# Performance work log

Measured on AMD Instinct MI355X. Metric: run time of the kernel, lower is better.

## Reference

```python
import jax, jax.numpy as jnp
import numpy as np

MASKED = True


def setup_inputs() -> dict:
    key = jax.random.key(0)
    kq, kk, kv = jax.random.split(key, 3)
    shape = (4, 16, 2048, 64)  # [B, H, S, d]
    q = jax.random.normal(kq, shape, dtype=jnp.float32)
    k = jax.random.normal(kk, shape, dtype=jnp.float32)
    v = jax.random.normal(kv, shape, dtype=jnp.float32)
    return {"q": q, "k": k, "v": v}


def reference(q, k, v):
    d = k.shape[-1]
    scale = 1.0 / jnp.sqrt(jnp.asarray(d, dtype=q.dtype))
    # [B, H, S, S]
    att = jnp.einsum("bhqd,bhkd->bhqk", q, k) * scale
    if MASKED:
        # Faithful to torch source: tril of the scores, then mask where zero
        tri = jnp.tril(att)
        att = jnp.where(tri == 0, -jnp.inf, att)
    att = jax.nn.softmax(att, axis=-1)
    return jnp.einsum("bhqk,bhkd->bhqd", att, v)
```

## Files before the change

kernel.cpp:

```cpp
#include <hip/hip_runtime.h>
#include <hip/hip_bf16.h>

typedef __attribute__((ext_vector_type(8)))  short bf16x8;
typedef __attribute__((ext_vector_type(4)))  float f32x4;
typedef __attribute__((ext_vector_type(16))) float f32x16;
typedef unsigned short ushort_t;

#define S_LEN 2048
#define D_DIM 64
#define FIXED_M 14.0f

#if __has_builtin(__builtin_amdgcn_exp2f)
#define EXP2(x) __builtin_amdgcn_exp2f(x)
#else
#define EXP2(x) __expf((x) * 0.6931471805599453f)
#endif

__device__ __forceinline__ short f2bf(float f) {
  union { float f; unsigned u; } x; x.f = f;
  unsigned r = x.u + 0x7fffu + ((x.u >> 16) & 1u);
  return (short)(r >> 16);
}

__device__ __forceinline__ unsigned cvtpk_bf16(float lo, float hi) {
  unsigned r;
  asm("v_cvt_pk_bf16_f32 %0, %1, %2" : "=v"(r) : "v"(lo), "v"(hi));
  return r;
}

__device__ __forceinline__ void pl32swap(unsigned& a, unsigned& b) {
  asm volatile("v_permlane32_swap_b32 %0, %1" : "+v"(a), "+v"(b));
}

__device__ __forceinline__ void gl_lds16(const ushort_t* g, ushort_t* l) {
  __builtin_amdgcn_global_load_lds(
      (const __attribute__((address_space(1))) unsigned*)g,
      (__attribute__((address_space(3))) unsigned*)l, 16, 0, 0);
}

__global__ void conv_bf16_kernel(const float* __restrict__ in,
                                 ushort_t* __restrict__ out, long n8) {
  long i = (long)blockIdx.x * blockDim.x + threadIdx.x;
  const long stride = (long)gridDim.x * blockDim.x;
  for (; i < n8; i += stride) {
    const float4* p = (const float4*)(in + i * 8);
    float4 a = p[0], b = p[1];
    bf16x8 t;
    t[0]=f2bf(a.x); t[1]=f2bf(a.y); t[2]=f2bf(a.z); t[3]=f2bf(a.w);
    t[4]=f2bf(b.x); t[5]=f2bf(b.y); t[6]=f2bf(b.z); t[7]=f2bf(b.w);
    *(bf16x8*)(out + i * 8) = t;
  }
}

__global__ void transpose_v_kernel(const float* __restrict__ V,
                                   ushort_t* __restrict__ Vt) {
  const int h  = blockIdx.x >> 5;
  const int s0 = (blockIdx.x & 31) * 64;
  const float* Vh = V + (size_t)h * S_LEN * D_DIM;
  ushort_t* Vth   = Vt + (size_t)h * D_DIM * S_LEN;
  __shared__ float tile[64][65];
  const int r  = threadIdx.x >> 2;
  const int c4 = (threadIdx.x & 3) * 16;
#pragma unroll
  for (int j = 0; j < 16; j += 4) {
    float4 x = *(const float4*)(Vh + (size_t)(s0 + r) * D_DIM + c4 + j);
    tile[r][c4 + j + 0] = x.x; tile[r][c4 + j + 1] = x.y;
    tile[r][c4 + j + 2] = x.z; tile[r][c4 + j + 3] = x.w;
  }
  __syncthreads();
  bf16x8 o0, o1;
#pragma unroll
  for (int j = 0; j < 8; ++j) o0[j] = f2bf(tile[c4 + j][r]);
#pragma unroll
  for (int j = 0; j < 8; ++j) o1[j] = f2bf(tile[c4 + 8 + j][r]);
  *(bf16x8*)(Vth + (size_t)r * S_LEN + s0 + c4)     = o0;
  *(bf16x8*)(Vth + (size_t)r * S_LEN + s0 + c4 + 8) = o1;
}

__global__ __launch_bounds__(256, 2)
void flash32_kernel(const float* __restrict__ Qf, const ushort_t* __restrict__ Kb,
                    const ushort_t* __restrict__ Vt, float* __restrict__ Og) {
  const int tid = threadIdx.x;
  const int l   = tid & 63;
  const int wv  = tid >> 6;
  const int hi  = l >> 5;
  const int l31 = l & 31;
  const int l7  = l & 7;
  const int l8  = l >> 3;

  const int bid  = blockIdx.x;
  const int r6   = bid & 63;
  const int head = (r6 & 7) * 8 + (r6 >> 3);
  const int g4   = bid >> 6;
  const int lo2  = g4 & 3;
  const int odd  = (g4 >> 2) & 1;
  const int top  = g4 >> 3;
  const int qidx = odd ? (top * 4 + lo2) : ((15 - top * 4) - lo2);
  const int q0   = qidx * 128;
  const int nt   = 2 * qidx + 2;

  const float*    Qh = Qf + (size_t)head * S_LEN * D_DIM;
  const ushort_t* Kh = Kb + (size_t)head * S_LEN * D_DIM;
  const ushort_t* Vh = Vt + (size_t)head * D_DIM * S_LEN;
  float*          Oh = Og + (size_t)head * S_LEN * D_DIM;

  __shared__ ushort_t smK[2][64 * 64];
  __shared__ ushort_t smV[2][64 * 64];

  const int qrow  = q0 + wv * 32 + l31;
  const int qminw = q0 + wv * 32;

  const int swsrc = (l7 ^ l8) * 8;
  const int rb    = l31 * 64;

#define STAGE_K(T, B) do {                                                 \
    const int kvk_ = (T) * 64;                                             \
    _Pragma("unroll")                                                      \
    for (int u_ = 0; u_ < 2; ++u_) {                                       \
      const int idx_ = wv * 2 + u_;                                        \
      const int row_ = idx_ * 8 + l8;                                      \
      gl_lds16(Kh + (size_t)(kvk_ + row_) * 64 + swsrc,                    \
               &smK[B][idx_ * 512]);                                       \
    }                                                                      \
  } while (0)

#define STAGE_V(T, B) do {                                                 \
    const int kvv_ = (T) * 64;                                             \
    _Pragma("unroll")                                                      \
    for (int u_ = 0; u_ < 2; ++u_) {                                       \
      const int idx_ = wv * 2 + u_;                                        \
      const int d_ = idx_ * 8 + l8;                                        \
      gl_lds16(Vh + (size_t)d_ * S_LEN + kvv_ + swsrc,                     \
               &smV[B][idx_ * 512]);                                       \
    }                                                                      \
  } while (0)

#define VMCNT0() asm volatile("s_waitcnt vmcnt(0)" ::: "memory")

#define QKT(S0, S1, KB) do {                                               \
    _Pragma("unroll")                                                      \
    for (int i = 0; i < 16; ++i) { S0[i] = 0.f; S1[i] = 0.f; }             \
    const ushort_t* kb_ = smK[KB];                                         \
    __builtin_amdgcn_s_setprio(1);                                         \
    _Pragma("unroll")                                                      \
    for (int ks = 0; ks < 4; ++ks) {                                       \
      const int ch = ((ks * 2 + hi) ^ l7) * 8;                             \
      bf16x8 a0 = *(const bf16x8*)(kb_ + rb + ch);                         \
      bf16x8 a1 = *(const bf16x8*)(kb_ + 2048 + rb + ch);                  \
      S0 = __builtin_amdgcn_mfma_f32_32x32x16_bf16(a0, qf[ks], S0, 0, 0, 0); \
      S1 = __builtin_amdgcn_mfma_f32_32x32x16_bf16(a1, qf[ks], S1, 0, 0, 0); \
    }                                                                      \
    __builtin_amdgcn_s_setprio(0);                                         \
  } while (0)

#define SOFTMAX(S0, S1, KV0) do {                                          \
    if ((KV0) + 63 > qminw) {                                              \
      _Pragma("unroll")                                                    \
      for (int r = 0; r < 16; ++r) {                                       \
        const int crow = (r & 3) + 8 * (r >> 2) + 4 * hi;                  \
        if ((KV0) + crow > qrow)      S0[r] = -INFINITY;                   \
        if ((KV0) + 32 + crow > qrow) S1[r] = -INFINITY;                   \
      }                                                                    \
    }                                                                      \
    _Pragma("unroll")                                                      \
    for (int i = 0; i < 16; ++i) S0[i] = EXP2(S0[i] - FIXED_M);            \
    _Pragma("unroll")                                                      \
    for (int i = 0; i < 16; ++i) S1[i] = EXP2(S1[i] - FIXED_M);            \
    float b8[8];                                                           \
    _Pragma("unroll")                                                      \
    for (int i = 0; i < 8; ++i)                                            \
      b8[i] = (S0[i] + S0[i+8]) + (S1[i] + S1[i+8]);                       \
    _Pragma("unroll")                                                      \
    for (int i = 0; i < 4; ++i) b8[i] += b8[i+4];                          \
    l_run += (b8[0] + b8[2]) + (b8[1] + b8[3]);                            \
    _Pragma("unroll")                                                      \
    for (int ks = 0; ks < 4; ++ks) {                                       \
      const int r0 = (ks & 1) * 8;                                         \
      unsigned w0, w1, w2, w3;                                             \
      if (ks < 2) {                                                        \
        w0 = cvtpk_bf16(S0[r0+0], S0[r0+1]); w2 = cvtpk_bf16(S0[r0+4], S0[r0+5]); \
        w1 = cvtpk_bf16(S0[r0+2], S0[r0+3]); w3 = cvtpk_bf16(S0[r0+6], S0[r0+7]); \
      } else {                                                             \
        w0 = cvtpk_bf16(S1[r0+0], S1[r0+1]); w2 = cvtpk_bf16(S1[r0+4], S1[r0+5]); \
        w1 = cvtpk_bf16(S1[r0+2], S1[r0+3]); w3 = cvtpk_bf16(S1[r0+6], S1[r0+7]); \
      }                                                                    \
      pl32swap(w0, w2); pl32swap(w1, w3);                                  \
      union { unsigned u[4]; bf16x8 v; } pu_;                              \
      pu_.u[0] = w0; pu_.u[1] = w1; pu_.u[2] = w2; pu_.u[3] = w3;          \
      pw[ks] = pu_.v;                                                      \
    }                                                                      \
  } while (0)

#define PV(VB) do {                                                        \
    const ushort_t* vb_ = smV[VB];                                         \
    __builtin_amdgcn_s_setprio(1);                                         \
    _Pragma("unroll")                                                      \
    for (int ks = 0; ks < 4; ++ks) {                                       \
      const int ch = ((ks * 2 + hi) ^ l7) * 8;                             \
      bf16x8 va  = *(const bf16x8*)(vb_ + rb + ch);                        \
      bf16x8 vB2 = *(const bf16x8*)(vb_ + 2048 + rb + ch);                 \
      accA = __builtin_amdgcn_mfma_f32_32x32x16_bf16(va,  pw[ks], accA, 0, 0, 0); \
      accB = __builtin_amdgcn_mfma_f32_32x32x16_bf16(vB2, pw[ks], accB, 0, 0, 0); \
    }                                                                      \
    __builtin_amdgcn_s_setprio(0);                                         \
  } while (0)

  STAGE_K(0, 0);
  STAGE_V(0, 0);
  STAGE_K(1, 1);

  bf16x8 qf[4];
  {
    const float sc = 0.125f * 1.44269504089f;
    const float* qp = Qh + (size_t)qrow * D_DIM + 8 * hi;
#pragma unroll
    for (int ks = 0; ks < 4; ++ks) {
      float4 x = *(const float4*)(qp + ks * 16);
      float4 y = *(const float4*)(qp + ks * 16 + 4);
      bf16x8 t;
      t[0]=f2bf(x.x*sc); t[1]=f2bf(x.y*sc);
      t[2]=f2bf(x.z*sc); t[3]=f2bf(x.w*sc);
      t[4]=f2bf(y.x*sc); t[5]=f2bf(y.y*sc);
      t[6]=f2bf(y.z*sc); t[7]=f2bf(y.w*sc);
      qf[ks] = t;
    }
  }

  f32x16 accA, accB, sA0, sA1, sB0, sB1;
#pragma unroll
  for (int i = 0; i < 16; ++i) { accA[i] = 0.f; accB[i] = 0.f; }
  float l_run = 0.f;
  bf16x8 pw[4];

  VMCNT0();
  __builtin_amdgcn_s_barrier();
  QKT(sA0, sA1, 0);

  for (int t = 0; t + 2 < nt; t += 2) {
    VMCNT0();
    __builtin_amdgcn_s_barrier();
    STAGE_K(t + 2, 0);
    STAGE_V(t + 1, 1);
    QKT(sB0, sB1, 1);
    SOFTMAX(sA0, sA1, t * 64);
    PV(0);
    VMCNT0();
    __builtin_amdgcn_s_barrier();
    STAGE_K(t + 3, 1);
    STAGE_V(t + 2, 0);
    QKT(sA0, sA1, 0);
    SOFTMAX(sB0, sB1, (t + 1) * 64);
    PV(1);
  }

  VMCNT0();
  __builtin_amdgcn_s_barrier();
  STAGE_V(nt - 1, 1);
  QKT(sB0, sB1, 1);
  SOFTMAX(sA0, sA1, (nt - 2) * 64);
  PV(0);
  VMCNT0();
  __builtin_amdgcn_s_barrier();
  SOFTMAX(sB0, sB1, (nt - 1) * 64);
  PV(1);

#undef STAGE_K
#undef STAGE_V
#undef VMCNT0
#undef QKT
#undef SOFTMAX
#undef PV

  l_run += __shfl_xor(l_run, 32, 64);
  const float inv = 1.0f / l_run;
  float* op = Oh + (size_t)qrow * D_DIM + 4 * hi;
#pragma unroll
  for (int m4 = 0; m4 < 4; ++m4) {
    float4 a = { accA[4*m4+0]*inv, accA[4*m4+1]*inv,
                 accA[4*m4+2]*inv, accA[4*m4+3]*inv };
    *(float4*)(op + 8 * m4) = a;
    float4 b = { accB[4*m4+0]*inv, accB[4*m4+1]*inv,
                 accB[4*m4+2]*inv, accB[4*m4+3]*inv };
    *(float4*)(op + 32 + 8 * m4) = b;
  }
}

#define BQ 64
#define BK 64
#define LDK 72
#define LDP 72

__device__ __forceinline__ unsigned pack_bf(float lo, float hi) {
  return (unsigned)(unsigned short)f2bf(lo) |
         ((unsigned)(unsigned short)f2bf(hi) << 16);
}

__global__ __launch_bounds__(256, 2)
void flash_fwd_kernel(const float* __restrict__ Qg, const float* __restrict__ Kg,
                      const float* __restrict__ Vg, float* __restrict__ Og) {
  const int tid  = threadIdx.x;
  const int lane = tid & 63;
  const int wv   = tid >> 6;
  const int grp  = lane >> 4;
  const int l16  = lane & 15;
  const int bid = blockIdx.x;
  const int qb  = 31 - (bid & 31);
  const int bh  = bid >> 5;
  const int q0  = qb * BQ;
  const size_t hoff = (size_t)bh * S_LEN * D_DIM;
  const float* Qh = Qg + hoff;
  const float* Kh = Kg + hoff;
  const float* Vh = Vg + hoff;
  float*       Oh = Og + hoff;
  __shared__ short sK [BK][LDK];
  __shared__ short sVT[D_DIM][LDP];
  __shared__ short sP [4][16][LDP];
  bf16x8 qf[2];
  {
    const float* qrow = Qh + (size_t)(q0 + wv*16 + l16) * D_DIM + grp*8;
#pragma unroll
    for (int kc = 0; kc < 2; ++kc) {
      float4 a = *reinterpret_cast<const float4*>(qrow + kc*32);
      float4 b = *reinterpret_cast<const float4*>(qrow + kc*32 + 4);
      bf16x8 t;
      t[0]=f2bf(a.x*0.125f); t[1]=f2bf(a.y*0.125f);
      t[2]=f2bf(a.z*0.125f); t[3]=f2bf(a.w*0.125f);
      t[4]=f2bf(b.x*0.125f); t[5]=f2bf(b.y*0.125f);
      t[6]=f2bf(b.z*0.125f); t[7]=f2bf(b.w*0.125f);
      qf[kc] = t;
    }
  }
  f32x4 acc[4];
#pragma unroll
  for (int nb = 0; nb < 4; ++nb) acc[nb] = (f32x4){0.f, 0.f, 0.f, 0.f};
  float m_i[4] = {-INFINITY, -INFINITY, -INFINITY, -INFINITY};
  float l_i[4] = {0.f, 0.f, 0.f, 0.f};
  const int srow = tid >> 2;
  const int scb  = tid & 3;
  for (int kt = 0; kt <= qb; ++kt) {
    const int kv0 = kt * BK;
    __syncthreads();
    {
      const float* src = Kh + (size_t)(kv0 + srow) * D_DIM + scb*16;
      float4 x0 = *reinterpret_cast<const float4*>(src);
      float4 x1 = *reinterpret_cast<const float4*>(src + 4);
      float4 x2 = *reinterpret_cast<const float4*>(src + 8);
      float4 x3 = *reinterpret_cast<const float4*>(src + 12);
      bf16x8 lo, hi;
      lo[0]=f2bf(x0.x); lo[1]=f2bf(x0.y); lo[2]=f2bf(x0.z); lo[3]=f2bf(x0.w);
      lo[4]=f2bf(x1.x); lo[5]=f2bf(x1.y); lo[6]=f2bf(x1.z); lo[7]=f2bf(x1.w);
      hi[0]=f2bf(x2.x); hi[1]=f2bf(x2.y); hi[2]=f2bf(x2.z); hi[3]=f2bf(x2.w);
      hi[4]=f2bf(x3.x); hi[5]=f2bf(x3.y); hi[6]=f2bf(x3.z); hi[7]=f2bf(x3.w);
      *reinterpret_cast<bf16x8*>(&sK[srow][scb*16])     = lo;
      *reinterpret_cast<bf16x8*>(&sK[srow][scb*16 + 8]) = hi;
    }
    {
      const float* src = Vh + (size_t)(kv0 + scb*16) * D_DIM + srow;
      bf16x8 lo, hi;
#pragma unroll
      for (int j = 0; j < 8; ++j) lo[j] = f2bf(src[(size_t)j * D_DIM]);
#pragma unroll
      for (int j = 0; j < 8; ++j) hi[j] = f2bf(src[(size_t)(j + 8) * D_DIM]);
      *reinterpret_cast<bf16x8*>(&sVT[srow][scb*16])     = lo;
      *reinterpret_cast<bf16x8*>(&sVT[srow][scb*16 + 8]) = hi;
    }
    __syncthreads();
    f32x4 sc[4];
#pragma unroll
    for (int nb = 0; nb < 4; ++nb) {
      f32x4 c = (f32x4){0.f, 0.f, 0.f, 0.f};
#pragma unroll
      for (int kc = 0; kc < 2; ++kc) {
        bf16x8 kf = *reinterpret_cast<const bf16x8*>(&sK[nb*16 + l16][kc*32 + grp*8]);
        c = __builtin_amdgcn_mfma_f32_16x16x32_bf16(qf[kc], kf, c, 0, 0, 0);
      }
      sc[nb] = c;
    }
    const bool diag = (kt == qb);
#pragma unroll
    for (int r = 0; r < 4; ++r) {
      const int qi = wv*16 + grp*4 + r;
      float s0 = sc[0][r], s1 = sc[1][r], s2 = sc[2][r], s3 = sc[3][r];
      if (diag) {
        if (l16 +  0 > qi) s0 = -INFINITY;
        if (l16 + 16 > qi) s1 = -INFINITY;
        if (l16 + 32 > qi) s2 = -INFINITY;
        if (l16 + 48 > qi) s3 = -INFINITY;
      }
      float mx = fmaxf(fmaxf(s0, s1), fmaxf(s2, s3));
#pragma unroll
      for (int off = 8; off; off >>= 1)
        mx = fmaxf(mx, __shfl_xor(mx, off, 64));
      const float mn    = fmaxf(m_i[r], mx);
      const float alpha = __expf(m_i[r] - mn);
      const float p0 = __expf(s0 - mn);
      const float p1 = __expf(s1 - mn);
      const float p2 = __expf(s2 - mn);
      const float p3 = __expf(s3 - mn);
      float rs = (p0 + p1) + (p2 + p3);
#pragma unroll
      for (int off = 8; off; off >>= 1)
        rs += __shfl_xor(rs, off, 64);
      l_i[r] = l_i[r] * alpha + rs;
      m_i[r] = mn;
      acc[0][r] *= alpha; acc[1][r] *= alpha;
      acc[2][r] *= alpha; acc[3][r] *= alpha;
      const float n0 = __shfl_xor(p0, 1, 64);
      const float n1 = __shfl_xor(p1, 1, 64);
      const float n2 = __shfl_xor(p2, 1, 64);
      const float n3 = __shfl_xor(p3, 1, 64);
      if (!(lane & 1)) {
        const int prow = grp*4 + r;
        unsigned* base = reinterpret_cast<unsigned*>(&sP[wv][prow][l16]);
        base[0]  = pack_bf(p0, n0);
        base[8]  = pack_bf(p1, n1);
        base[16] = pack_bf(p2, n2);
        base[24] = pack_bf(p3, n3);
      }
    }
    bf16x8 pf[2];
#pragma unroll
    for (int kc = 0; kc < 2; ++kc)
      pf[kc] = *reinterpret_cast<const bf16x8*>(&sP[wv][l16][kc*32 + grp*8]);
#pragma unroll
    for (int nb = 0; nb < 4; ++nb) {
#pragma unroll
      for (int kc = 0; kc < 2; ++kc) {
        bf16x8 vf = *reinterpret_cast<const bf16x8*>(&sVT[l16 + 16*nb][kc*32 + grp*8]);
        acc[nb] = __builtin_amdgcn_mfma_f32_16x16x32_bf16(pf[kc], vf, acc[nb], 0, 0, 0);
      }
    }
  }
#pragma unroll
  for (int r = 0; r < 4; ++r) {
    const float inv = 1.0f / l_i[r];
    float* orow = Oh + (size_t)(q0 + wv*16 + grp*4 + r) * D_DIM + l16;
#pragma unroll
    for (int nb = 0; nb < 4; ++nb)
      orow[nb*16] = acc[nb][r] * inv;
  }
}

extern "C" void kernel_launch(void* const* d_in, const int* in_sizes, int n_in,
                              void* d_out, int out_size, void* d_ws, size_t ws_size,
                              hipStream_t stream) {
  (void)n_in; (void)out_size;
  const float* q = (const float*)d_in[0];
  const float* k = (const float*)d_in[1];
  const float* v = (const float*)d_in[2];
  float* o = (float*)d_out;
  const int bh = in_sizes[0] / (S_LEN * D_DIM);
  const size_t elems = (size_t)bh * S_LEN * D_DIM;

  if (ws_size >= elems * 2 * 2) {
    ushort_t* Kb = (ushort_t*)d_ws;
    ushort_t* Vt = Kb + elems;
    const long n8 = (long)(elems / 8);
    conv_bf16_kernel<<<2048, 256, 0, stream>>>(k, Kb, n8);
    transpose_v_kernel<<<bh * (S_LEN / 64), 256, 0, stream>>>(v, Vt);
    flash32_kernel<<<bh * (S_LEN / 128), 256, 0, stream>>>(q, Kb, Vt, o);
  } else {
    flash_fwd_kernel<<<bh * (S_LEN / BQ), 256, 0, stream>>>(q, k, v, o);
  }
}
```

Measured before the change: 78.52 us.

## Restructure attention loop to process two KV tiles per barrier with 4-slot LDS

```diff
diff --git a/kernel.cpp b/kernel.cpp
--- a/kernel.cpp
+++ b/kernel.cpp
@@ -104,8 +104,8 @@
   const ushort_t* Vh = Vt + (size_t)head * D_DIM * S_LEN;
   float*          Oh = Og + (size_t)head * S_LEN * D_DIM;
 
-  __shared__ ushort_t smK[2][64 * 64];
-  __shared__ ushort_t smV[2][64 * 64];
+  __shared__ ushort_t smK[4][64 * 64];
+  __shared__ ushort_t smV[4][64 * 64];
 
   const int qrow  = q0 + wv * 32 + l31;
   const int qminw = q0 + wv * 32;
@@ -113,34 +113,36 @@
   const int swsrc = (l7 ^ l8) * 8;
   const int rb    = l31 * 64;
 
-#define STAGE_K(T, B) do {                                                 \
+#define STAGE_K(T) do {                                                    \
     const int kvk_ = (T) * 64;                                             \
+    ushort_t* dst_ = smK[(T) & 3];                                         \
     _Pragma("unroll")                                                      \
     for (int u_ = 0; u_ < 2; ++u_) {                                       \
       const int idx_ = wv * 2 + u_;                                        \
       const int row_ = idx_ * 8 + l8;                                      \
       gl_lds16(Kh + (size_t)(kvk_ + row_) * 64 + swsrc,                    \
-               &smK[B][idx_ * 512]);                                       \
+               dst_ + idx_ * 512);                                         \
     }                                                                      \
   } while (0)
 
-#define STAGE_V(T, B) do {                                                 \
+#define STAGE_V(T) do {                                                    \
     const int kvv_ = (T) * 64;                                             \
+    ushort_t* dst_ = smV[(T) & 3];                                         \
     _Pragma("unroll")                                                      \
     for (int u_ = 0; u_ < 2; ++u_) {                                       \
       const int idx_ = wv * 2 + u_;                                        \
       const int d_ = idx_ * 8 + l8;                                        \
       gl_lds16(Vh + (size_t)d_ * S_LEN + kvv_ + swsrc,                     \
-               &smV[B][idx_ * 512]);                                       \
+               dst_ + idx_ * 512);                                         \
     }                                                                      \
   } while (0)
 
 #define VMCNT0() asm volatile("s_waitcnt vmcnt(0)" ::: "memory")
 
-#define QKT(S0, S1, KB) do {                                               \
+#define QKT(S0, S1, T) do {                                                \
     _Pragma("unroll")                                                      \
     for (int i = 0; i < 16; ++i) { S0[i] = 0.f; S1[i] = 0.f; }             \
-    const ushort_t* kb_ = smK[KB];                                         \
+    const ushort_t* kb_ = smK[(T) & 3];                                    \
     __builtin_amdgcn_s_setprio(1);                                         \
     _Pragma("unroll")                                                      \
     for (int ks = 0; ks < 4; ++ks) {                                       \
@@ -153,7 +155,7 @@
     __builtin_amdgcn_s_setprio(0);                                         \
   } while (0)
 
-#define SOFTMAX(S0, S1, KV0) do {                                          \
+#define SOFTMAX(S0, S1, KV0, PW) do {                                      \
     if ((KV0) + 63 > qminw) {                                              \
       _Pragma("unroll")                                                    \
       for (int r = 0; r < 16; ++r) {                                       \
@@ -187,27 +189,28 @@
       pl32swap(w0, w2); pl32swap(w1, w3);                                  \
       union { unsigned u[4]; bf16x8 v; } pu_;                              \
       pu_.u[0] = w0; pu_.u[1] = w1; pu_.u[2] = w2; pu_.u[3] = w3;          \
-      pw[ks] = pu_.v;                                                      \
+      PW[ks] = pu_.v;                                                      \
     }                                                                      \
   } while (0)
 
-#define PV(VB) do {                                                        \
-    const ushort_t* vb_ = smV[VB];                                         \
+#define PV(T, PW) do {                                                     \
+    const ushort_t* vb_ = smV[(T) & 3];                                    \
     __builtin_amdgcn_s_setprio(1);                                         \
     _Pragma("unroll")                                                      \
     for (int ks = 0; ks < 4; ++ks) {                                       \
       const int ch = ((ks * 2 + hi) ^ l7) * 8;                             \
       bf16x8 va  = *(const bf16x8*)(vb_ + rb + ch);                        \
       bf16x8 vB2 = *(const bf16x8*)(vb_ + 2048 + rb + ch);                 \
-      accA = __builtin_amdgcn_mfma_f32_32x32x16_bf16(va,  pw[ks], accA, 0, 0, 0); \
-      accB = __builtin_amdgcn_mfma_f32_32x32x16_bf16(vB2, pw[ks], accB, 0, 0, 0); \
+      accA = __builtin_amdgcn_mfma_f32_32x32x16_bf16(va,  PW[ks], accA, 0, 0, 0); \
+      accB = __builtin_amdgcn_mfma_f32_32x32x16_bf16(vB2, PW[ks], accB, 0, 0, 0); \
     }                                                                      \
     __builtin_amdgcn_s_setprio(0);                                         \
   } while (0)
 
-  STAGE_K(0, 0);
-  STAGE_V(0, 0);
-  STAGE_K(1, 1);
+  STAGE_K(0);
+  STAGE_V(0);
+  STAGE_K(1);
+  STAGE_V(1);
 
   bf16x8 qf[4];
   {
@@ -230,39 +233,27 @@
 #pragma unroll
   for (int i = 0; i < 16; ++i) { accA[i] = 0.f; accB[i] = 0.f; }
   float l_run = 0.f;
-  bf16x8 pw[4];
+  bf16x8 pwA[4], pwB[4];
 
   VMCNT0();
   __builtin_amdgcn_s_barrier();
-  QKT(sA0, sA1, 0);
-
-  for (int t = 0; t + 2 < nt; t += 2) {
+
+  for (int t = 0; t < nt; t += 2) {
+    if (t + 2 < nt) {
+      STAGE_K(t + 2);
+      STAGE_V(t + 2);
+      STAGE_K(t + 3);
+      STAGE_V(t + 3);
+    }
+    QKT(sA0, sA1, t);
+    QKT(sB0, sB1, t + 1);
+    SOFTMAX(sA0, sA1, t * 64, pwA);
+    SOFTMAX(sB0, sB1, (t + 1) * 64, pwB);
+    PV(t, pwA);
+    PV(t + 1, pwB);
     VMCNT0();
     __builtin_amdgcn_s_barrier();
-    STAGE_K(t + 2, 0);
-    STAGE_V(t + 1, 1);
-    QKT(sB0, sB1, 1);
-    SOFTMAX(sA0, sA1, t * 64);
-    PV(0);
-    VMCNT0();
-    __builtin_amdgcn_s_barrier();
-    STAGE_K(t + 3, 1);
-    STAGE_V(t + 2, 0);
-    QKT(sA0, sA1, 0);
-    SOFTMAX(sB0, sB1, (t + 1) * 64);
-    PV(1);
-  }
-
-  VMCNT0();
-  __builtin_amdgcn_s_barrier();
-  STAGE_V(nt - 1, 1);
-  QKT(sB0, sB1, 1);
-  SOFTMAX(sA0, sA1, (nt - 2) * 64);
-  PV(0);
-  VMCNT0();
-  __builtin_amdgcn_s_barrier();
-  SOFTMAX(sB0, sB1, (nt - 1) * 64);
-  PV(1);
+  }
 
 #undef STAGE_K
 #undef STAGE_V
```

Measured after the change: 80.86 us. 3.0% more time.

## Pair causal query tiles per block, merge prep kernels, fold max offset into init

Applied to the files above, without the earlier changes.

```diff
diff --git a/kernel.cpp b/kernel.cpp
--- a/kernel.cpp
+++ b/kernel.cpp
@@ -38,43 +38,44 @@
       (__attribute__((address_space(3))) unsigned*)l, 16, 0, 0);
 }
 
-__global__ void conv_bf16_kernel(const float* __restrict__ in,
-                                 ushort_t* __restrict__ out, long n8) {
-  long i = (long)blockIdx.x * blockDim.x + threadIdx.x;
-  const long stride = (long)gridDim.x * blockDim.x;
-  for (; i < n8; i += stride) {
-    const float4* p = (const float4*)(in + i * 8);
-    float4 a = p[0], b = p[1];
-    bf16x8 t;
-    t[0]=f2bf(a.x); t[1]=f2bf(a.y); t[2]=f2bf(a.z); t[3]=f2bf(a.w);
-    t[4]=f2bf(b.x); t[5]=f2bf(b.y); t[6]=f2bf(b.z); t[7]=f2bf(b.w);
-    *(bf16x8*)(out + i * 8) = t;
-  }
-}
-
-__global__ void transpose_v_kernel(const float* __restrict__ V,
-                                   ushort_t* __restrict__ Vt) {
-  const int h  = blockIdx.x >> 5;
-  const int s0 = (blockIdx.x & 31) * 64;
-  const float* Vh = V + (size_t)h * S_LEN * D_DIM;
-  ushort_t* Vth   = Vt + (size_t)h * D_DIM * S_LEN;
-  __shared__ float tile[64][65];
-  const int r  = threadIdx.x >> 2;
-  const int c4 = (threadIdx.x & 3) * 16;
-#pragma unroll
-  for (int j = 0; j < 16; j += 4) {
-    float4 x = *(const float4*)(Vh + (size_t)(s0 + r) * D_DIM + c4 + j);
-    tile[r][c4 + j + 0] = x.x; tile[r][c4 + j + 1] = x.y;
-    tile[r][c4 + j + 2] = x.z; tile[r][c4 + j + 3] = x.w;
-  }
-  __syncthreads();
-  bf16x8 o0, o1;
-#pragma unroll
-  for (int j = 0; j < 8; ++j) o0[j] = f2bf(tile[c4 + j][r]);
-#pragma unroll
-  for (int j = 0; j < 8; ++j) o1[j] = f2bf(tile[c4 + 8 + j][r]);
-  *(bf16x8*)(Vth + (size_t)r * S_LEN + s0 + c4)     = o0;
-  *(bf16x8*)(Vth + (size_t)r * S_LEN + s0 + c4 + 8) = o1;
+__global__ void prep_kernel(const float* __restrict__ Kf, const float* __restrict__ Vf,
+                            ushort_t* __restrict__ Kb, ushort_t* __restrict__ Vt) {
+  if (blockIdx.x < 2048) {
+    const long n8 = (long)64 * S_LEN * D_DIM / 8;
+    long i = (long)blockIdx.x * blockDim.x + threadIdx.x;
+    const long stride = (long)2048 * blockDim.x;
+    for (; i < n8; i += stride) {
+      const float4* p = (const float4*)(Kf + i * 8);
+      float4 a = p[0], b = p[1];
+      bf16x8 t;
+      t[0]=f2bf(a.x); t[1]=f2bf(a.y); t[2]=f2bf(a.z); t[3]=f2bf(a.w);
+      t[4]=f2bf(b.x); t[5]=f2bf(b.y); t[6]=f2bf(b.z); t[7]=f2bf(b.w);
+      *(bf16x8*)(Kb + i * 8) = t;
+    }
+  } else {
+    const int bid = blockIdx.x - 2048;
+    const int h  = bid >> 5;
+    const int s0 = (bid & 31) * 64;
+    const float* Vh = Vf + (size_t)h * S_LEN * D_DIM;
+    ushort_t* Vth   = Vt + (size_t)h * D_DIM * S_LEN;
+    __shared__ float tile[64][65];
+    const int r  = threadIdx.x >> 2;
+    const int c4 = (threadIdx.x & 3) * 16;
+#pragma unroll
+    for (int j = 0; j < 16; j += 4) {
+      float4 x = *(const float4*)(Vh + (size_t)(s0 + r) * D_DIM + c4 + j);
+      tile[r][c4 + j + 0] = x.x; tile[r][c4 + j + 1] = x.y;
+      tile[r][c4 + j + 2] = x.z; tile[r][c4 + j + 3] = x.w;
+    }
+    __syncthreads();
+    bf16x8 o0, o1;
+#pragma unroll
+    for (int j = 0; j < 8; ++j) o0[j] = f2bf(tile[c4 + j][r]);
+#pragma unroll
+    for (int j = 0; j < 8; ++j) o1[j] = f2bf(tile[c4 + 8 + j][r]);
+    *(bf16x8*)(Vth + (size_t)r * S_LEN + s0 + c4)     = o0;
+    *(bf16x8*)(Vth + (size_t)r * S_LEN + s0 + c4 + 8) = o1;
+  }
 }
 
 __global__ __launch_bounds__(256, 2)
@@ -91,13 +92,9 @@
   const int bid  = blockIdx.x;
   const int r6   = bid & 63;
   const int head = (r6 & 7) * 8 + (r6 >> 3);
-  const int g4   = bid >> 6;
-  const int lo2  = g4 & 3;
-  const int odd  = (g4 >> 2) & 1;
-  const int top  = g4 >> 3;
-  const int qidx = odd ? (top * 4 + lo2) : ((15 - top * 4) - lo2);
-  const int q0   = qidx * 128;
-  const int nt   = 2 * qidx + 2;
+  const int p    = bid >> 6;
+  const int qhiQ = 15 - p;
+  const int qloQ = p;
 
   const float*    Qh = Qf + (size_t)head * S_LEN * D_DIM;
   const ushort_t* Kh = Kb + (size_t)head * S_LEN * D_DIM;
@@ -106,9 +103,6 @@
 
   __shared__ ushort_t smK[2][64 * 64];
   __shared__ ushort_t smV[2][64 * 64];
-
-  const int qrow  = q0 + wv * 32 + l31;
-  const int qminw = q0 + wv * 32;
 
   const int swsrc = (l7 ^ l8) * 8;
   const int rb    = l31 * 64;
@@ -136,10 +130,11 @@
   } while (0)
 
 #define VMCNT0() asm volatile("s_waitcnt vmcnt(0)" ::: "memory")
+#define BAR()    __builtin_amdgcn_s_barrier()
 
 #define QKT(S0, S1, KB) do {                                               \
     _Pragma("unroll")                                                      \
-    for (int i = 0; i < 16; ++i) { S0[i] = 0.f; S1[i] = 0.f; }             \
+    for (int i = 0; i < 16; ++i) { S0[i] = -FIXED_M; S1[i] = -FIXED_M; }   \
     const ushort_t* kb_ = smK[KB];                                         \
     __builtin_amdgcn_s_setprio(1);                                         \
     _Pragma("unroll")                                                      \
@@ -163,9 +158,9 @@
       }                                                                    \
     }                                                                      \
     _Pragma("unroll")                                                      \
-    for (int i = 0; i < 16; ++i) S0[i] = EXP2(S0[i] - FIXED_M);            \
-    _Pragma("unroll")                                                      \
-    for (int i = 0; i < 16; ++i) S1[i] = EXP2(S1[i] - FIXED_M);            \
+    for (int i = 0; i < 16; ++i) S0[i] = EXP2(S0[i]);                      \
+    _Pragma("unroll")                                                      \
+    for (int i = 0; i < 16; ++i) S1[i] = EXP2(S1[i]);                      \
     float b8[8];                                                           \
     _Pragma("unroll")                                                      \
     for (int i = 0; i < 8; ++i)                                            \
@@ -205,84 +200,94 @@
     __builtin_amdgcn_s_setprio(0);                                         \
   } while (0)
 
-  STAGE_K(0, 0);
-  STAGE_V(0, 0);
-  STAGE_K(1, 1);
-
-  bf16x8 qf[4];
-  {
-    const float sc = 0.125f * 1.44269504089f;
-    const float* qp = Qh + (size_t)qrow * D_DIM + 8 * hi;
-#pragma unroll
-    for (int ks = 0; ks < 4; ++ks) {
-      float4 x = *(const float4*)(qp + ks * 16);
-      float4 y = *(const float4*)(qp + ks * 16 + 4);
-      bf16x8 t;
-      t[0]=f2bf(x.x*sc); t[1]=f2bf(x.y*sc);
-      t[2]=f2bf(x.z*sc); t[3]=f2bf(x.w*sc);
-      t[4]=f2bf(y.x*sc); t[5]=f2bf(y.y*sc);
-      t[6]=f2bf(y.z*sc); t[7]=f2bf(y.w*sc);
-      qf[ks] = t;
-    }
-  }
-
-  f32x16 accA, accB, sA0, sA1, sB0, sB1;
-#pragma unroll
-  for (int i = 0; i < 16; ++i) { accA[i] = 0.f; accB[i] = 0.f; }
-  float l_run = 0.f;
-  bf16x8 pw[4];
-
-  VMCNT0();
-  __builtin_amdgcn_s_barrier();
-  QKT(sA0, sA1, 0);
-
-  for (int t = 0; t + 2 < nt; t += 2) {
+  for (int seg = 0; seg < 2; ++seg) {
+    const int qidx = seg ? qloQ : qhiQ;
+    const int q0   = qidx * 128;
+    const int nt   = 2 * qidx + 2;
+
+    const int qrow  = q0 + wv * 32 + l31;
+    const int qminw = q0 + wv * 32;
+
+    if (seg) BAR();
+
+    STAGE_K(0, 0);
+    STAGE_V(0, 0);
+    STAGE_K(1, 1);
+
+    bf16x8 qf[4];
+    {
+      const float sc = 0.125f * 1.44269504089f;
+      const float* qp = Qh + (size_t)qrow * D_DIM + 8 * hi;
+#pragma unroll
+      for (int ks = 0; ks < 4; ++ks) {
+        float4 x = *(const float4*)(qp + ks * 16);
+        float4 y = *(const float4*)(qp + ks * 16 + 4);
+        bf16x8 t;
+        t[0]=f2bf(x.x*sc); t[1]=f2bf(x.y*sc);
+        t[2]=f2bf(x.z*sc); t[3]=f2bf(x.w*sc);
+        t[4]=f2bf(y.x*sc); t[5]=f2bf(y.y*sc);
+        t[6]=f2bf(y.z*sc); t[7]=f2bf(y.w*sc);
+        qf[ks] = t;
+      }
+    }
+
+    f32x16 accA, accB, sA0, sA1, sB0, sB1;
+#pragma unroll
+    for (int i = 0; i < 16; ++i) { accA[i] = 0.f; accB[i] = 0.f; }
+    float l_run = 0.f;
+    bf16x8 pw[4];
+
     VMCNT0();
-    __builtin_amdgcn_s_barrier();
-    STAGE_K(t + 2, 0);
-    STAGE_V(t + 1, 1);
-    QKT(sB0, sB1, 1);
-    SOFTMAX(sA0, sA1, t * 64);
-    PV(0);
-    VMCNT0();
-    __builtin_amdgcn_s_barrier();
-    STAGE_K(t + 3, 1);
-    STAGE_V(t + 2, 0);
+    BAR();
     QKT(sA0, sA1, 0);
-    SOFTMAX(sB0, sB1, (t + 1) * 64);
-    PV(1);
-  }
-
-  VMCNT0();
-  __builtin_amdgcn_s_barrier();
-  STAGE_V(nt - 1, 1);
-  QKT(sB0, sB1, 1);
-  SOFTMAX(sA0, sA1, (nt - 2) * 64);
-  PV(0);
-  VMCNT0();
-  __builtin_amdgcn_s_barrier();
-  SOFTMAX(sB0, sB1, (nt - 1) * 64);
-  PV(1);
+
+    for (int t = 0; t + 2 < nt; t += 2) {
+      VMCNT0(); BAR();
+      STAGE_K(t + 2, 0);
+      STAGE_V(t + 1, 1);
+      QKT(sB0, sB1, 1);
+      SOFTMAX(sA0, sA1, t * 64);
+      PV(0);
+      VMCNT0(); BAR();
+      STAGE_K(t + 3, 1);
+      STAGE_V(t + 2, 0);
+      QKT(sA0, sA1, 0);
+      SOFTMAX(sB0, sB1, (t + 1) * 64);
+      PV(1);
+    }
+    {
+      const int t = nt - 2;
+      VMCNT0(); BAR();
+      STAGE_V(t + 1, 1);
+      QKT(sB0, sB1, 1);
+      SOFTMAX(sA0, sA1, t * 64);
+      PV(0);
+      VMCNT0(); BAR();
+      SOFTMAX(sB0, sB1, (t + 1) * 64);
+      PV(1);
+    }
+
+    l_run += __shfl_xor(l_run, 32, 64);
+    const float inv = 1.0f / l_run;
+    float* op = Oh + (size_t)qrow * D_DIM + 4 * hi;
+#pragma unroll
+    for (int m4 = 0; m4 < 4; ++m4) {
+      float4 a = { accA[4*m4+0]*inv, accA[4*m4+1]*inv,
+                   accA[4*m4+2]*inv, accA[4*m4+3]*inv };
+      *(float4*)(op + 8 * m4) = a;
+      float4 b = { accB[4*m4+0]*inv, accB[4*m4+1]*inv,
+                   accB[4*m4+2]*inv, accB[4*m4+3]*inv };
+      *(float4*)(op + 32 + 8 * m4) = b;
+    }
+  }
 
 #undef STAGE_K
 #undef STAGE_V
 #undef VMCNT0
+#undef BAR
 #undef QKT
 #undef SOFTMAX
 #undef PV
-
-  l_run += __shfl_xor(l_run, 32, 64);
-  const float inv = 1.0f / l_run;
-  float* op = Oh + (size_t)qrow * D_DIM + 4 * hi;
-#pragma unroll
-  for (int m4 = 0; m4 < 4; ++m4) {
-    float4 a = { accA[4*m4+0]*inv, accA[4*m4+1]*inv,
-                 accA[4*m4+2]*inv, accA[4*m4+3]*inv };
-    *(float4*)(op + 8 * m4) = a;
-    float4 b = { accB[4*m4+0]*inv, accB[4*m4+1]*inv,
-                 accB[4*m4+2]*inv, accB[4*m4+3]*inv };
-    *(float4*)(op + 32 + 8 * m4) = b;
-  }
 }
 
 #define BQ 64
@@ -452,13 +457,11 @@
   const int bh = in_sizes[0] / (S_LEN * D_DIM);
   const size_t elems = (size_t)bh * S_LEN * D_DIM;
 
-  if (ws_size >= elems * 2 * 2) {
+  if (ws_size >= elems * 2 * 2 && bh == 64) {
     ushort_t* Kb = (ushort_t*)d_ws;
     ushort_t* Vt = Kb + elems;
-    const long n8 = (long)(elems / 8);
-    conv_bf16_kernel<<<2048, 256, 0, stream>>>(k, Kb, n8);
-    transpose_v_kernel<<<bh * (S_LEN / 64), 256, 0, stream>>>(v, Vt);
-    flash32_kernel<<<bh * (S_LEN / 128), 256, 0, stream>>>(q, Kb, Vt, o);
+    prep_kernel<<<4096, 256, 0, stream>>>(k, v, Kb, Vt);
+    flash32_kernel<<<bh * 8, 256, 0, stream>>>(q, Kb, Vt, o);
   } else {
     flash_fwd_kernel<<<bh * (S_LEN / BQ), 256, 0, stream>>>(q, k, v, o);
   }
```

Result: faster. 70.45 us (median of 2 runs) (-10.3%).
